# Kernel tuning notes

Hardware: AMD Instinct MI355X
Metric: run time of the kernel (lower is better)

## Reference

```python
import jax, jax.numpy as jnp
import numpy as np

NLAYERS, NHEADS, NFEAT, HDIM = 2, 8, 512, 64
ALPHA = 0.2
NEG = -9e15


def setup_inputs() -> dict:
    key = jax.random.key(0)
    ks = jax.random.split(key, 20)
    B, Ng, Nc, Nq = 4, 1024, 1024, 256
    s = 0.05
    inp = {
        "gloss": jax.random.normal(ks[0], (B, Ng, NFEAT), jnp.float32),
        "clip": jax.random.normal(ks[1], (B, Nc, NFEAT), jnp.float32),
        "question": jax.random.normal(ks[2], (B, Nq, NFEAT), jnp.float32),
        "gloss2clipadj": jax.random.randint(ks[3], (B, Ng, Nc), 0, 2, jnp.int32),
        "gloss2questionadj": jax.random.randint(ks[4], (B, Ng, Nq), 0, 2, jnp.int32),
    }
    # per-layer, per-head attention params: W [L,H,F,D], a split halves a1/a2 [L,H,D]
    for i, name in enumerate(["c2g", "g2q", "q2g"]):
        inp[name + "_W"] = jax.random.normal(ks[5 + i], (NLAYERS, NHEADS, NFEAT, HDIM), jnp.float32) * s
        inp[name + "_a1"] = jax.random.normal(ks[8 + i], (NLAYERS, NHEADS, HDIM), jnp.float32) * s
        inp[name + "_a2"] = jax.random.normal(ks[11 + i], (NLAYERS, NHEADS, HDIM), jnp.float32) * s
    # 4 FusionLayers per encoder layer (G2C, C2G, G2Q, Q2G), each with W,U,Wf,Uf [F,F]
    for i, name in enumerate(["fus_W", "fus_U", "fus_Wf", "fus_Uf"]):
        inp[name] = jax.random.normal(ks[14 + i], (NLAYERS, 4, NFEAT, NFEAT), jnp.float32) * s
    return inp


def _attn(q, kv, adj, W, a1, a2):
    # multi-head GAT-style additive cross attention; W [H,F,D], q [B,N,F], kv [B,M,F], adj [B,N,M]
    Wq = jnp.einsum('bnf,hfd->bhnd', q, W)
    Wk = jnp.einsum('bmf,hfd->bhmd', kv, W)
    e = jax.nn.leaky_relu(
        jnp.einsum('bhnd,hd->bhn', Wq, a1)[:, :, :, None]
        + jnp.einsum('bhmd,hd->bhm', Wk, a2)[:, :, None, :], ALPHA)
    e = jnp.where(adj[:, None, :, :] > 0, e, NEG)
    att = jax.nn.softmax(e, axis=2)  # torch F.softmax(dim=1) on [B,N,M]: query axis (faithful)
    h = jax.nn.elu(jnp.einsum('bhnm,bhmd->bhnd', att, Wk))
    B, H, N, D = h.shape
    return jnp.transpose(h, (0, 2, 1, 3)).reshape(B, N, H * D)  # concat heads


def _fusion(a, b, W, U, Wf, Uf):
    new_a = a @ W + b @ U
    f = jax.nn.sigmoid(a @ Wf + b @ Uf)
    return f * new_a + (1.0 - f) * a  # dropout is identity at inference


def reference(gloss, clip, question, gloss2clipadj, gloss2questionadj,
              c2g_W, c2g_a1, c2g_a2, g2q_W, g2q_a1, g2q_a2, q2g_W, q2g_a1, q2g_a2,
              fus_W, fus_U, fus_Wf, fus_Uf):
    g2c_f = gloss2clipadj.astype(gloss.dtype)
    g2q_T = jnp.transpose(gloss2questionadj, (0, 2, 1))
    for l in range(NLAYERS):
        gloss_same = jnp.einsum('bnm,bnf->bmf', g2c_f, gloss)  # adj^T @ gloss
        clip_1 = _fusion(clip, gloss_same, fus_W[l, 0], fus_U[l, 0], fus_Wf[l, 0], fus_Uf[l, 0])
        clip_agg = _attn(gloss, clip, gloss2clipadj, c2g_W[l], c2g_a1[l], c2g_a2[l])
        gloss_1 = _fusion(gloss, clip_agg, fus_W[l, 1], fus_U[l, 1], fus_Wf[l, 1], fus_Uf[l, 1])
        gloss_agg = _attn(question, gloss, g2q_T, g2q_W[l], g2q_a1[l], g2q_a2[l])
        question_1 = _fusion(question, gloss_agg, fus_W[l, 2], fus_U[l, 2], fus_Wf[l, 2], fus_Uf[l, 2])
        question_agg = _attn(gloss, question, gloss2questionadj, q2g_W[l], q2g_a1[l], q2g_a2[l])
        gloss_2 = _fusion(gloss_1, question_agg, fus_W[l, 3], fus_U[l, 3], fus_Wf[l, 3], fus_Uf[l, 3])
        gloss, clip, question = gloss_2, clip_1, question_1
    return gloss, clip, question
```

## Files before the change

kernel.cpp:

```cpp
#include <hip/hip_runtime.h>
#include <math.h>

#define NFEAT 512
#define NHEADS 8
#define HDIM 64
#define NB 4
#define NG 1024
#define NC 1024
#define NQ 256
#define NEGV -9e15f
#define CHUNKS 16
#define FF ((size_t)NFEAT*NFEAT)
#define LSTR 36
#define SEG 2304

typedef _Float16 v8h __attribute__((ext_vector_type(8)));
typedef float v4f __attribute__((ext_vector_type(4)));
#define MFMA16(a,b,c) __builtin_amdgcn_mfma_f32_16x16x32_f16((a),(b),(c),0,0,0)

#define GLDS(g, l) __builtin_amdgcn_global_load_lds( \
    (__attribute__((address_space(1))) void*)(g), \
    (__attribute__((address_space(3))) void*)(l), 16, 0, 0)

__device__ __forceinline__ int ldsw(int row, int quad){
// ... 119 lines not shown
    int b = blockIdx.z;
    int c0 = blockIdx.x*64, g0 = blockIdx.y*64;
    __shared__ int sI[64][65];
    int tid = threadIdx.x;
    #pragma unroll
    for (int it = 0; it < 4; ++it){
        int idx = it*256 + tid;
        int r = idx >> 4, c4 = idx & 15;
        int4 v = *(const int4*)(adj + ((size_t)b*NG + g0 + r)*NC + c0 + c4*4);
        sI[r][c4*4+0]=v.x; sI[r][c4*4+1]=v.y; sI[r][c4*4+2]=v.z; sI[r][c4*4+3]=v.w;
    }
    __syncthreads();
    int wv = tid >> 6, lane = tid & 63;
    #pragma unroll
    for (int it = 0; it < 2; ++it){
        int idx = it*256 + tid;
        int dd = idx >> 3, c8 = idx & 7;
        ushort4 p0, p1;
        #pragma unroll
        for (int j = 0; j < 4; ++j) (&p0.x)[j] = sI[c8*8+j][dd] > 0 ? (unsigned short)0x3C00 : (unsigned short)0;
        #pragma unroll
        for (int j = 0; j < 4; ++j) (&p1.x)[j] = sI[c8*8+4+j][dd] > 0 ? (unsigned short)0x3C00 : (unsigned short)0;
        unsigned short* o = dst + ((size_t)b*NC + c0 + dd)*NG + g0 + c8*8;
        *(ushort4*)o = p0; *(ushort4*)(o+4) = p1;
    }
    #pragma unroll
    for (int rr = wv; rr < 64; rr += 4){
        unsigned long long m = __ballot(sI[rr][lane] > 0);
        if (lane == 0) bm_gc[((size_t)b*NG + g0 + rr)*(NC/64) + (c0>>6)] = m;
    }
    #pragma unroll
    for (int cc = wv; cc < 64; cc += 4){
        unsigned long long m = __ballot(sI[lane][cc] > 0);
        if (lane == 0) bm_cg[((size_t)b*NC + c0 + cc)*(NG/64) + (g0>>6)] = m;
    }
}

__global__ __launch_bounds__(256) void adjT_int_k(const int* __restrict__ adj, int* __restrict__ dst,
    unsigned long long* __restrict__ bm_gq, unsigned long long* __restrict__ bm_qg){
    int b = blockIdx.z;
    int q0 = blockIdx.x*64, g0 = blockIdx.y*64;
    __shared__ int sI[64][65];
    int tid = threadIdx.x;
    #pragma unroll
    for (int it = 0; it < 4; ++it){
        int idx = it*256 + tid;
        int r = idx >> 4, c4 = idx & 15;
        int4 v = *(const int4*)(adj + ((size_t)b*NG + g0 + r)*NQ + q0 + c4*4);
        sI[r][c4*4+0]=v.x; sI[r][c4*4+1]=v.y; sI[r][c4*4+2]=v.z; sI[r][c4*4+3]=v.w;
    }
    __syncthreads();
    int wv = tid >> 6, lane = tid & 63;
    #pragma unroll
    for (int it = 0; it < 4; ++it){
        int idx = it*256 + tid;
        int dd = idx >> 4, c4 = idx & 15;
        int4 v{sI[c4*4+0][dd], sI[c4*4+1][dd], sI[c4*4+2][dd], sI[c4*4+3][dd]};
        *(int4*)(dst + ((size_t)b*NQ + q0 + dd)*NG + g0 + c4*4) = v;
    }
    #pragma unroll
    for (int rr = wv; rr < 64; rr += 4){
        unsigned long long m = __ballot(sI[rr][lane] > 0);
        if (lane == 0) bm_gq[((size_t)b*NG + g0 + rr)*(NQ/64) + (q0>>6)] = m;
    }
    #pragma unroll
    for (int cc = wv; cc < 64; cc += 4){
        unsigned long long m = __ballot(sI[lane][cc] > 0);
        if (lane == 0) bm_qg[((size_t)b*NQ + q0 + cc)*(NG/64) + (g0>>6)] = m;
    }
}

__global__ __launch_bounds__(256) void actT_hl_k(const float* __restrict__ src,
    unsigned short* __restrict__ dstHi, unsigned short* __restrict__ dstLo,
    unsigned short* __restrict__ rmHi, unsigned short* __restrict__ rmLo, int Nrows){
    int b = blockIdx.z;
    int f0 = blockIdx.x*64, g0 = blockIdx.y*64;
    __shared__ float sF[64][65];
    int tid = threadIdx.x;
    #pragma unroll
    for (int it = 0; it < 4; ++it){
        int idx = it*256 + tid;
        int r = idx >> 4, c4 = idx & 15;
        float4 v = *(const float4*)(src + ((size_t)b*Nrows + g0 + r)*512 + f0 + c4*4);
        sF[r][c4*4+0]=v.x; sF[r][c4*4+1]=v.y; sF[r][c4*4+2]=v.z; sF[r][c4*4+3]=v.w;
    }
    __syncthreads();
    #pragma unroll
    for (int it = 0; it < 2; ++it){
        int idx = it*256 + tid;
        int dd = idx >> 3, c8 = idx & 7;
        unsigned short hi[8], lo[8];
        #pragma unroll
        for (int j = 0; j < 8; ++j){
            float x = sF[c8*8+j][dd];
            hi[j] = f2h(x);
            lo[j] = f2h(x - h2f(hi[j]));
        }
        size_t oo = ((size_t)b*512 + f0 + dd)*Nrows + g0 + c8*8;
        *(ushort4*)(dstHi+oo)   = ushort4{hi[0],hi[1],hi[2],hi[3]};
        *(ushort4*)(dstHi+oo+4) = ushort4{hi[4],hi[5],hi[6],hi[7]};
        *(ushort4*)(dstLo+oo)   = ushort4{lo[0],lo[1],lo[2],lo[3]};
        *(ushort4*)(dstLo+oo+4) = ushort4{lo[4],lo[5],lo[6],lo[7]};
    }
    #pragma unroll
    for (int it = 0; it < 2; ++it){
        int idx = it*256 + tid;
        int r = idx >> 3, c8 = idx & 7;
        unsigned short hi[8], lo[8];
        #pragma unroll
        for (int j = 0; j < 8; ++j){
            float x = sF[r][c8*8+j];
            hi[j] = f2h(x);
            lo[j] = f2h(x - h2f(hi[j]));
        }
        size_t oo = ((size_t)b*Nrows + g0 + r)*512 + f0 + c8*8;
        *(ushort4*)(rmHi+oo)   = ushort4{hi[0],hi[1],hi[2],hi[3]};
        *(ushort4*)(rmHi+oo+4) = ushort4{hi[4],hi[5],hi[6],hi[7]};
        *(ushort4*)(rmLo+oo)   = ushort4{lo[0],lo[1],lo[2],lo[3]};
        *(ushort4*)(rmLo+oo+4) = ushort4{lo[4],lo[5],lo[6],lo[7]};
    }
}

__global__ __launch_bounds__(256) void scores3_k(
    const unsigned short* __restrict__ g, const unsigned short* __restrict__ c,
    const unsigned short* __restrict__ q,
    const float* __restrict__ wa13, const float* __restrict__ wa23,
    float* __restrict__ qs3, float* __restrict__ ks3){
    int lane = threadIdx.x & 63;
    int grow = blockIdx.x*4 + (threadIdx.x >> 6);
    int b = grow / 4608; int r = grow - b*4608;
    const unsigned short* X; const float* wa; float* out; int n, oOff, rowsX;
    if (r < SEG){
        out = qs3;
        if (r < 1024)      { X=g; wa=wa13;        n=r;        oOff=0;    rowsX=NG; }
        else if (r < 1280) { X=q; wa=wa13+4096;   n=r-1024;   oOff=1024; rowsX=NQ; }
        else               { X=g; wa=wa13+8192;   n=r-1280;   oOff=1280; rowsX=NG; }
    } else {
        out = ks3; r -= SEG;
        if (r < 1024)      { X=c; wa=wa23;        n=r;        oOff=0;    rowsX=NC; }
        else if (r < 2048) { X=g; wa=wa23+4096;   n=r-1024;   oOff=1024; rowsX=NG; }
        else               { X=q; wa=wa23+8192;   n=r-2048;   oOff=2048; rowsX=NQ; }
    }
    const unsigned short* Xr = X + ((size_t)b*rowsX + n)*NFEAT;
    float p[NHEADS];
    #pragma unroll
    for (int h = 0; h < NHEADS; ++h) p[h] = 0.f;
    #pragma unroll
    for (int cc = 0; cc < 8; ++cc){
        float x = h2f(Xr[(cc<<6) + lane]);
        #pragma unroll
        for (int h = 0; h < NHEADS; ++h) p[h] += x * wa[(h<<9) + (cc<<6) + lane];
    }
    #pragma unroll
    for (int h = 0; h < NHEADS; ++h){
        float v = p[h];
        #pragma unroll
        for (int off = 32; off > 0; off >>= 1) v += __shfl_xor(v, off);
        if (lane == 0) out[((size_t)b*SEG + oOff + n)*8 + h] = v;
    }
}

__global__ __launch_bounds__(256) void wkt3_mfma_k(
    const unsigned short* __restrict__ c, const unsigned short* __restrict__ g,
    const unsigned short* __restrict__ q, const unsigned short* __restrict__ WT3,
    unsigned short* __restrict__ WkT3){
    int b = blockIdx.z;
    int y = blockIdx.y;
    const unsigned short* kv; int rowsX, mOff, a;
    if (y < 16)      { a=0; kv=c; rowsX=NC; mOff=0; }
    else if (y < 32) { a=1; y-=16; kv=g; rowsX=NG; mOff=1024; }
    else             { a=2; y-=32; kv=q; rowsX=NQ; mOff=2048; }
    int r0 = y*64, c0 = blockIdx.x*64;
    int tid = threadIdx.x;
    __shared__ alignas(16) unsigned short aS[2][2048], bS[2][2048];
    const unsigned short* aG = kv + (size_t)b*rowsX*512;
    const unsigned short* bG = WT3 + (size_t)a*FF;
    int w = tid >> 6, lane = tid & 63;
    int lrow = lane & 15, quad = lane >> 4;
    int sr = tid >> 2;
    int sq = (tid & 3) ^ ((sr >> 1) & 3);
    size_t aRow = (size_t)(r0 + sr)*512 + sq*8;
    size_t bRow = (size_t)(c0 + sr)*512 + sq*8;
    v4f acc[4];
    #pragma unroll
    for (int cf = 0; cf < 4; ++cf) acc[cf] = (v4f)0.f;
    GLDS(aG + aRow, &aS[0][w << 9]);
    GLDS(bG + bRow, &bS[0][w << 9]);
    __syncthreads();
    int buf = 0;
    for (int s = 0; s < 16; ++s){
        if (s < 15){
            int ktn = (s + 1) << 5;
            GLDS(aG + aRow + ktn, &aS[buf^1][w << 9]);
            GLDS(bG + bRow + ktn, &bS[buf^1][w << 9]);
        }
        v8h af = *(const v8h*)&aS[buf][ldsw(w*16 + lrow, quad)];
        #pragma unroll
        for (int cf = 0; cf < 4; ++cf){
            v8h bf = *(const v8h*)&bS[buf][ldsw(cf*16 + lrow, quad)];
            acc[cf] = MFMA16(af, bf, acc[cf]);
        }
        __syncthreads();
        buf ^= 1;
    }
    #pragma unroll
    for (int cf = 0; cf < 4; ++cf){
        int colg = c0 + cf*16 + lrow;
        int rbase = r0 + w*16 + quad*4;
        ushort4 pk{f2h(acc[cf][0]), f2h(acc[cf][1]), f2h(acc[cf][2]), f2h(acc[cf][3])};
        *(ushort4*)&WkT3[((size_t)b*512 + colg)*SEG + mOff + rbase] = pk;
    }
}

__global__ __launch_bounds__(256) void colstat3_k(
    const unsigned* __restrict__ bm_cg, const unsigned* __restrict__ bm_gq,
    const unsigned* __restrict__ bm_qg,
    const float* __restrict__ qs3, const float* __restrict__ ks3,
    float* __restrict__ pcm, float* __restrict__ psum){
    int x = blockIdx.x, b = blockIdx.z;
    const unsigned* bm; int Mrows, N, N32, mOff, qOff;
    if (x < 256)      { bm=bm_cg; Mrows=NC; N=NG; N32=NG/32; mOff=0;    qOff=0; }
    else if (x < 512) { x-=256; bm=bm_gq; Mrows=NG; N=NQ; N32=NQ/32; mOff=1024; qOff=1024; }
    else              { x-=512; bm=bm_qg; Mrows=NQ; N=NG; N32=NG/32; mOff=2048; qOff=1280; }
    int mt = x >> 4, ch = x & 15;
    int chunk = N / CHUNKS, subl = chunk >> 2;
    int ml = threadIdx.x & 63; int m = mt*64 + ml;
    int g = threadIdx.x >> 6;
    int n0 = ch*chunk + g*subl;
    __shared__ float sQ[64][8];
    for (int t2 = threadIdx.x; t2 < chunk*8; t2 += 256)
        sQ[t2>>3][t2&7] = qs3[((size_t)b*SEG + qOff + ch*chunk)*8 + t2];
    float ksv[8];
    size_t mo = ((size_t)b*SEG + mOff + m)*8;
    #pragma unroll
    for (int h = 0; h < 8; ++h) ksv[h] = ks3[mo+h];
    unsigned word = bm[((size_t)b*Mrows + m)*N32 + (n0>>5)];
    unsigned bits = (word >> (n0 & 31)) & ((1u << subl) - 1u);
    __syncthreads();
    int nb = g*subl;
    float mx[8];
    #pragma unroll
    for (int h = 0; h < 8; ++h) mx[h] = -INFINITY;
    for (int i = 0; i < subl; ++i){
        if ((bits >> i) & 1){
            #pragma unroll
            for (int h = 0; h < 8; ++h) mx[h] = fmaxf(mx[h], sQ[nb+i][h]);
        }
    }
    float cm[8], s[8];
    #pragma unroll
    for (int h = 0; h < 8; ++h){
        cm[h] = bits ? lrelu(mx[h] + ksv[h]) : NEGV;
        s[h] = 0.f;
    }
    for (int i = 0; i < subl; ++i){
        bool on = (bits >> i) & 1;
        #pragma unroll
        for (int h = 0; h < 8; ++h){
            float e = on ? lrelu(sQ[nb+i][h] + ksv[h]) : NEGV;
            s[h] += __expf(e - cm[h]);
        }
    }
    __shared__ float scm[4][64][8], ssm[4][64][8];
    #pragma unroll
    for (int h = 0; h < 8; ++h){ scm[g][ml][h] = cm[h]; ssm[g][ml][h] = s[h]; }
    __syncthreads();
    if (g == 0){
        #pragma unroll
        for (int h = 0; h < 8; ++h){
            float c0 = scm[0][ml][h], c1 = scm[1][ml][h], c2 = scm[2][ml][h], c3 = scm[3][ml][h];
            float CM = fmaxf(fmaxf(c0, c1), fmaxf(c2, c3));
            float S = ssm[0][ml][h]*__expf(c0-CM) + ssm[1][ml][h]*__expf(c1-CM)
                    + ssm[2][ml][h]*__expf(c2-CM) + ssm[3][ml][h]*__expf(c3-CM);
            size_t o = (((size_t)b*CHUNKS + ch)*SEG + mOff + m)*8 + h;
            pcm[o] = CM; psum[o] = S;
        }
    }
}

__global__ __launch_bounds__(256) void colfin3_k(const float* __restrict__ pcm, const float* __restrict__ psum,
    const float* __restrict__ ks3, float* __restrict__ ksh, float* __restrict__ cmh,
    float* __restrict__ ish){
    int idx = blockIdx.x*256 + threadIdx.x;
    const int m8 = SEG*8;
    int b = idx / m8, rem = idx - b*m8;
    int m = rem >> 3, h = rem & 7;
    size_t base = (size_t)b*CHUNKS*m8 + rem;
    float c[CHUNKS], s[CHUNKS];
    #pragma unroll
    for (int ch = 0; ch < CHUNKS; ++ch){
        c[ch] = pcm[base + (size_t)ch*m8];
        s[ch] = psum[base + (size_t)ch*m8];
    }
    float CM = c[0];
    #pragma unroll
    for (int ch = 1; ch < CHUNKS; ++ch) CM = fmaxf(CM, c[ch]);
    float S = 0.f;
    #pragma unroll
    for (int ch = 0; ch < CHUNKS; ++ch) S += s[ch]*__expf(c[ch] - CM);
    size_t o = ((size_t)b*8 + h)*SEG + m;
    ksh[o] = ks3[idx]; cmh[o] = CM; ish[o] = 1.f/S;
}

__global__ __launch_bounds__(256) void fusion3_k(
    const unsigned short* __restrict__ aHi, const unsigned short* __restrict__ aLo,
    const unsigned short* __restrict__ bHi, const unsigned short* __restrict__ bLo,
    const unsigned short* __restrict__ Whi, const unsigned short* __restrict__ Wlo,
    unsigned short* __restrict__ dst, unsigned short* __restrict__ dstLo,
    unsigned short* __restrict__ dstT, unsigned short* __restrict__ dstTLo,
    float* __restrict__ dstF, int rows){
    int nY = rows >> 6;
    int ppg = (nY * NB) >> 3;
    int F = blockIdx.x;
    int xcd = F & 7, t = F >> 3;
    int c0i = t / ppg;
    int p = xcd + ((t - c0i*ppg) << 3);
    int r0 = (p % nY) << 6, c0 = c0i << 6;
    int b = p / nY;
    int tid = threadIdx.x;
    __shared__ alignas(16) unsigned short aHs[2048], bHs[2048], aLs[2048], bLs[2048];
    __shared__ alignas(16) unsigned short wHs[8192], wLs[8192];
    size_t actOff = (size_t)b*rows*512;
    const unsigned short* aHG = aHi + actOff;
    const unsigned short* bHG = bHi + actOff;
    const unsigned short* aLG = aLo ? aLo + actOff : nullptr;
    const unsigned short* bLG = bLo ? bLo + actOff : nullptr;
    bool hasALo = (aLG != nullptr);
    bool hasBLo = (bLG != nullptr);
    int w = tid >> 6, lane = tid & 63;
    int wr = w >> 1, wc = w & 1;
    int lrow = lane & 15, quad = lane >> 4;
    int sr = tid >> 2;
    int sq = (tid & 3) ^ ((sr >> 1) & 3);
    size_t aRow = (size_t)(r0 + sr)*512 + sq*8;
    size_t wPk = (size_t)c0i*16*8192 + (size_t)sr*32 + sq*8;
    unsigned short* ldsA  = &aHs[w << 9];
    unsigned short* ldsB  = &bHs[w << 9];
    unsigned short* ldsAL = &aLs[w << 9];
    unsigned short* ldsBL = &bLs[w << 9];
    v4f accN[2][2], accF[2][2];
    #pragma unroll
    for (int r = 0; r < 2; ++r)
        #pragma unroll
        for (int cf = 0; cf < 2; ++cf){ accN[r][cf] = (v4f)0.f; accF[r][cf] = (v4f)0.f; }
    for (int kt = 0; kt < 512; kt += 32){
        __syncthreads();
        GLDS(aHG + aRow + kt, ldsA);
        GLDS(bHG + aRow + kt, ldsB);
        if (hasALo) GLDS(aLG + aRow + kt, ldsAL);
        if (hasBLo) GLDS(bLG + aRow + kt, ldsBL);
        size_t wk = wPk + (size_t)(kt >> 5)*8192;
        #pragma unroll
        for (int m = 0; m < 4; ++m){
            GLDS(Whi + wk + (m<<11), &wHs[(m<<11) + (w<<9)]);
            GLDS(Wlo + wk + (m<<11), &wLs[(m<<11) + (w<<9)]);
        }
        __syncthreads();
        v8h ah[2], bh[2], al[2], bl[2];
        #pragma unroll
        for (int r = 0; r < 2; ++r){
            int ao = ldsw(wr*32 + r*16 + lrow, quad);
            ah[r] = *(const v8h*)&aHs[ao];
            bh[r] = *(const v8h*)&bHs[ao];
            if (hasALo) al[r] = *(const v8h*)&aLs[ao];
            if (hasBLo) bl[r] = *(const v8h*)&bLs[ao];
        }
        #pragma unroll
        for (int cf = 0; cf < 2; ++cf){
            int wo = ldsw(wc*32 + cf*16 + lrow, quad);
            v8h w0 = *(const v8h*)&wHs[wo];
            v8h w1 = *(const v8h*)&wHs[2048 + wo];
            v8h w2 = *(const v8h*)&wHs[4096 + wo];
            v8h w3 = *(const v8h*)&wHs[6144 + wo];
            v8h l0 = *(const v8h*)&wLs[wo];
            v8h l1 = *(const v8h*)&wLs[2048 + wo];
            v8h l2 = *(const v8h*)&wLs[4096 + wo];
            v8h l3 = *(const v8h*)&wLs[6144 + wo];
            #pragma unroll
            for (int r = 0; r < 2; ++r){
                accN[r][cf] = MFMA16(ah[r], w0, accN[r][cf]);
                accN[r][cf] = MFMA16(bh[r], w1, accN[r][cf]);
                accF[r][cf] = MFMA16(ah[r], w2, accF[r][cf]);
                accF[r][cf] = MFMA16(bh[r], w3, accF[r][cf]);
                if (hasALo){ accN[r][cf] = MFMA16(al[r], w0, accN[r][cf]); accF[r][cf] = MFMA16(al[r], w2, accF[r][cf]); }
                if (hasBLo){ accN[r][cf] = MFMA16(bl[r], w1, accN[r][cf]); accF[r][cf] = MFMA16(bl[r], w3, accF[r][cf]); }
                accN[r][cf] = MFMA16(ah[r], l0, accN[r][cf]);
                accN[r][cf] = MFMA16(bh[r], l1, accN[r][cf]);
                accF[r][cf] = MFMA16(ah[r], l2, accF[r][cf]);
                accF[r][cf] = MFMA16(bh[r], l3, accF[r][cf]);
            }
        }
    }
    #pragma unroll
    for (int r = 0; r < 2; ++r)
        #pragma unroll
        for (int cf = 0; cf < 2; ++cf){
            int colg = c0 + wc*32 + cf*16 + lrow;
            int rbase = r0 + wr*32 + r*16 + quad*4;
            float o4[4];
            #pragma unroll
            for (int reg = 0; reg < 4; ++reg){
                float f = 1.f/(1.f + __expf(-accF[r][cf][reg]));
                size_t ai = (size_t)(rbase+reg)*512 + colg;
                float ao = h2f(aHG[ai]);
                if (aLG) ao += h2f(aLG[ai]);
                o4[reg] = f*accN[r][cf][reg] + (1.f - f)*ao;
                size_t oo = ((size_t)b*rows + rbase + reg)*512 + colg;
                unsigned short hv = f2h(o4[reg]);
                dst[oo] = hv;
                if (dstLo) dstLo[oo] = f2h(o4[reg] - h2f(hv));
                if (dstF) dstF[oo] = o4[reg];
            }
            if (dstT){
                unsigned short h0 = f2h(o4[0]), h1 = f2h(o4[1]), h2 = f2h(o4[2]), h3 = f2h(o4[3]);
                size_t to = ((size_t)b*512 + colg)*rows + rbase;
                *(ushort4*)&dstT[to] = ushort4{h0,h1,h2,h3};
                if (dstTLo)
                    *(ushort4*)&dstTLo[to] = ushort4{f2h(o4[0]-h2f(h0)), f2h(o4[1]-h2f(h1)),
                                                     f2h(o4[2]-h2f(h2)), f2h(o4[3]-h2f(h3))};
            }
        }
}

__global__ __launch_bounds__(256) void fusion1_k(
    const unsigned short* __restrict__ aHi, const unsigned short* __restrict__ aLo,
    const unsigned short* __restrict__ bHi,
    const unsigned short* __restrict__ Whi,
    unsigned short* __restrict__ dst, unsigned short* __restrict__ dstLo,
    float* __restrict__ dstF, int rows){
    int nY = rows >> 6;
    int ppg = (nY * NB) >> 3;
    int F = blockIdx.x;
    int xcd = F & 7, t = F >> 3;
    int c0i = t / ppg;
    int p = xcd + ((t - c0i*ppg) << 3);
    int r0 = (p % nY) << 6, c0 = c0i << 6;
    int b = p / nY;
    int tid = threadIdx.x;
    __shared__ alignas(16) unsigned short aHs[2][2048], bHs[2][2048];
    __shared__ alignas(16) unsigned short wHs[2][8192];
    size_t actOff = (size_t)b*rows*512;
    const unsigned short* aHG = aHi + actOff;
    const unsigned short* bHG = bHi + actOff;
    const unsigned short* aLG = aLo ? aLo + actOff : nullptr;
    int w = tid >> 6, lane = tid & 63;
    int wr = w >> 1, wc = w & 1;
    int lrow = lane & 15, quad = lane >> 4;
    int sr = tid >> 2;
    int sq = (tid & 3) ^ ((sr >> 1) & 3);
    size_t aRow = (size_t)(r0 + sr)*512 + sq*8;
    size_t wPk = (size_t)c0i*16*8192 + (size_t)sr*32 + sq*8;
    v4f accN[2][2], accF[2][2];
    #pragma unroll
    for (int r = 0; r < 2; ++r)
        #pragma unroll
        for (int cf = 0; cf < 2; ++cf){ accN[r][cf] = (v4f)0.f; accF[r][cf] = (v4f)0.f; }

    #define F1STAGE(bb, kk) do{ \
        GLDS(aHG + aRow + (kk), &aHs[bb][w << 9]); \
        GLDS(bHG + aRow + (kk), &bHs[bb][w << 9]); \
        size_t wk_ = wPk + (size_t)((kk) >> 5)*8192; \
        GLDS(Whi + wk_,          &wHs[bb][(0<<11) + (w<<9)]); \
        GLDS(Whi + wk_ + (1<<11), &wHs[bb][(1<<11) + (w<<9)]); \
        GLDS(Whi + wk_ + (2<<11), &wHs[bb][(2<<11) + (w<<9)]); \
        GLDS(Whi + wk_ + (3<<11), &wHs[bb][(3<<11) + (w<<9)]); \
    } while(0)

    F1STAGE(0, 0);
    __syncthreads();
    int buf = 0;
    for (int kt = 0; kt < 512; kt += 32){
        if (kt + 32 < 512) F1STAGE(buf^1, kt + 32);
        v8h ah[2], bh[2];
        #pragma unroll
        for (int r = 0; r < 2; ++r){
            int ao = ldsw(wr*32 + r*16 + lrow, quad);
            ah[r] = *(const v8h*)&aHs[buf][ao];
            bh[r] = *(const v8h*)&bHs[buf][ao];
        }
        #pragma unroll
        for (int cf = 0; cf < 2; ++cf){
            int wo = ldsw(wc*32 + cf*16 + lrow, quad);
            v8h w0 = *(const v8h*)&wHs[buf][wo];
            v8h w1 = *(const v8h*)&wHs[buf][2048 + wo];
            v8h w2 = *(const v8h*)&wHs[buf][4096 + wo];
            v8h w3 = *(const v8h*)&wHs[buf][6144 + wo];
            #pragma unroll
            for (int r = 0; r < 2; ++r){
                accN[r][cf] = MFMA16(ah[r], w0, accN[r][cf]);
                accN[r][cf] = MFMA16(bh[r], w1, accN[r][cf]);
                accF[r][cf] = MFMA16(ah[r], w2, accF[r][cf]);
                accF[r][cf] = MFMA16(bh[r], w3, accF[r][cf]);
            }
        }
        __syncthreads();
        buf ^= 1;
    }
    #undef F1STAGE
    #pragma unroll
    for (int r = 0; r < 2; ++r)
        #pragma unroll
        for (int cf = 0; cf < 2; ++cf){
            int colg = c0 + wc*32 + cf*16 + lrow;
            int rbase = r0 + wr*32 + r*16 + quad*4;
            #pragma unroll
            for (int reg = 0; reg < 4; ++reg){
                float f = 1.f/(1.f + __expf(-accF[r][cf][reg]));
                size_t ai = (size_t)(rbase+reg)*512 + colg;
                float ao = h2f(aHG[ai]);
                if (aLG) ao += h2f(aLG[ai]);
                float o = f*accN[r][cf][reg] + (1.f - f)*ao;
                size_t oo = ((size_t)b*rows + rbase + reg)*512 + colg;
                unsigned short hv = f2h(o);
                dst[oo] = hv;
                if (dstLo) dstLo[oo] = f2h(o - h2f(hv));
                if (dstF) dstF[oo] = o;
            }
        }
}

__global__ __launch_bounds__(256) void gemmT_mfma_k(
    const unsigned short* __restrict__ A, size_t aStride,
    const unsigned short* __restrict__ BT, const unsigned short* __restrict__ BT2, size_t bStride,
    int K, int rowsPB,
    unsigned short* __restrict__ outRM, unsigned short* __restrict__ outLo,
    unsigned short* __restrict__ outT){
    int b = blockIdx.z;
    int r0 = blockIdx.y*64, c0 = blockIdx.x*64;
    int tid = threadIdx.x;
    __shared__ alignas(16) unsigned short aS[2][2048], bS[2][2048];
    const unsigned short* aG = A + (size_t)b*aStride;
    const unsigned short* bG0 = BT + (size_t)b*bStride;
    const unsigned short* bG1 = BT2 ? BT2 + (size_t)b*bStride : nullptr;
    int w = tid >> 6, lane = tid & 63;
    int lrow = lane & 15, quad = lane >> 4;
    int sr = tid >> 2;
    int sq = (tid & 3) ^ ((sr >> 1) & 3);
    size_t aRow = (size_t)(r0 + sr)*K + sq*8;
    size_t bRow = (size_t)(c0 + sr)*K + sq*8;
    int spp = K >> 5;
    int nsteps = (BT2 ? 2 : 1)*spp;
    v4f acc[4];
    #pragma unroll
    for (int cf = 0; cf < 4; ++cf) acc[cf] = (v4f)0.f;
    GLDS(aG + aRow, &aS[0][w << 9]);
    GLDS(bG0 + bRow, &bS[0][w << 9]);
    __syncthreads();
    int buf = 0;
    for (int s = 0; s < nsteps; ++s){
        int sn = s + 1;
        if (sn < nsteps){
            int ktn = ((sn >= spp) ? (sn - spp) : sn) << 5;
            const unsigned short* bgn = (sn >= spp) ? bG1 : bG0;
            GLDS(aG + aRow + ktn, &aS[buf^1][w << 9]);
            GLDS(bgn + bRow + ktn, &bS[buf^1][w << 9]);
        }
        v8h af = *(const v8h*)&aS[buf][ldsw(w*16 + lrow, quad)];
        #pragma unroll
        for (int cf = 0; cf < 4; ++cf){
            v8h bf = *(const v8h*)&bS[buf][ldsw(cf*16 + lrow, quad)];
            acc[cf] = MFMA16(af, bf, acc[cf]);
        }
        __syncthreads();
        buf ^= 1;
    }
    #pragma unroll
    for (int cf = 0; cf < 4; ++cf){
        int colg = c0 + cf*16 + lrow;
        int rbase = r0 + w*16 + quad*4;
        if (outRM){
            #pragma unroll
            for (int reg = 0; reg < 4; ++reg){
                float v = acc[cf][reg];
                unsigned short hv = f2h(v);
                size_t oo = ((size_t)b*rowsPB + rbase + reg)*512 + colg;
                outRM[oo] = hv;
                if (outLo) outLo[oo] = f2h(v - h2f(hv));
            }
        }
        if (outT){
            ushort4 pk{f2h(acc[cf][0]), f2h(acc[cf][1]), f2h(acc[cf][2]), f2h(acc[cf][3])};
            *(ushort4*)&outT[((size_t)b*512 + colg)*rowsPB + rbase] = pk;
        }
    }
}

__global__ __launch_bounds__(256) void attn_mfma_k(const unsigned* __restrict__ bmN, int M32,
    const float* __restrict__ qs3, int qOff,
    const float* __restrict__ ksh, const float* __restrict__ cmh, const float* __restrict__ ish,
    int mOff, const unsigned short* __restrict__ WkT3,
    unsigned short* __restrict__ outp, int N, int M){
    int nN0 = N >> 6;
    int F = blockIdx.x;
    int xcd = F & 7, t = F >> 3;
    int bh = xcd*4 + t/nN0;
    int n0 = (t % nN0) << 6;
    int b = bh >> 3, h = bh & 7;
    int tid = threadIdx.x;
    __shared__ unsigned short pS[2*64*LSTR];
    __shared__ alignas(16) unsigned short wS[2*2048];
    __shared__ float qsS[64];
    __shared__ alignas(16) float sKs[1024], sCm[1024], sIs[1024];
    const float* ksb = ksh + ((size_t)b*8 + h)*SEG + mOff;
    const float* cmb = cmh + ((size_t)b*8 + h)*SEG + mOff;
    const float* isb = ish + ((size_t)b*8 + h)*SEG + mOff;
    const unsigned short* wkb = WkT3 + ((size_t)b*512 + h*64)*SEG + mOff;
    int w = tid >> 6, lane = tid & 63;
    int lrow = lane & 15, quad = lane >> 4;
    int pn = tid >> 2, pm = (tid & 3)*8;
    int sr = tid >> 2;
    int sq = (tid & 3) ^ ((sr >> 1) & 3);
    for (int o = w*256; o < M; o += 1024){
        GLDS(ksb + o + lane*4, &sKs[o]);
        GLDS(cmb + o + lane*4, &sCm[o]);
        GLDS(isb + o + lane*4, &sIs[o]);
    }
    if (tid < 64) qsS[tid] = qs3[((size_t)b*SEG + qOff + n0 + tid)*8 + h];
    const unsigned* bmrow = bmN + ((size_t)b*N + n0 + pn)*M32;
    v4f acc[4];
    #pragma unroll
    for (int cf = 0; cf < 4; ++cf) acc[cf] = (v4f)0.f;
    uint2 CW = *(const uint2*)(bmrow);
    uint2 NW;
    __syncthreads();
    float qv = qsS[pn];
    for (int mt = 0; mt < M; mt += 64){
        int mtB = mt + 32;
        int mtN = (mt + 64 < M) ? (mt + 64) : 0;
        GLDS(wkb + (size_t)sr*SEG + mt + sq*8, &wS[w << 9]);
        {
            unsigned bb = (CW.x >> pm) & 0xffu;
            float4 k0 = *(const float4*)&sKs[mt+pm], k1 = *(const float4*)&sKs[mt+pm+4];
            float4 c0 = *(const float4*)&sCm[mt+pm], c1 = *(const float4*)&sCm[mt+pm+4];
            float4 i0 = *(const float4*)&sIs[mt+pm], i1 = *(const float4*)&sIs[mt+pm+4];
            float p[8];
            const float* kk0 = &k0.x; const float* kk1 = &k1.x;
            const float* cc0 = &c0.x; const float* cc1 = &c1.x;
            const float* ii0 = &i0.x; const float* ii1 = &i1.x;
            #pragma unroll
            for (int j = 0; j < 4; ++j){
                float e = ((bb >> j) & 1) ? lrelu(qv + kk0[j]) : NEGV;
                p[j] = __expf(e - cc0[j]) * ii0[j];
            }
            #pragma unroll
            for (int j = 0; j < 4; ++j){
                float e = ((bb >> (4+j)) & 1) ? lrelu(qv + kk1[j]) : NEGV;
                p[4+j] = __expf(e - cc1[j]) * ii1[j];
            }
            *(ushort4*)&pS[pn*LSTR + pm]     = ushort4{f2h(p[0]), f2h(p[1]), f2h(p[2]), f2h(p[3])};
            *(ushort4*)&pS[pn*LSTR + pm + 4] = ushort4{f2h(p[4]), f2h(p[5]), f2h(p[6]), f2h(p[7])};
        }
        __syncthreads();
        {
            v8h af = *(const v8h*)&pS[(w*16 + lrow)*LSTR + quad*8];
            #pragma unroll
            for (int cf = 0; cf < 4; ++cf){
                v8h bf = *(const v8h*)&wS[ldsw(cf*16 + lrow, quad)];
                acc[cf] = MFMA16(af, bf, acc[cf]);
            }
        }
        GLDS(wkb + (size_t)sr*SEG + mtB + sq*8, &wS[2048 + (w << 9)]);
        NW = *(const uint2*)(bmrow + (mtN >> 5));
        {
            unsigned bb = (CW.y >> pm) & 0xffu;
            float4 k0 = *(const float4*)&sKs[mtB+pm], k1 = *(const float4*)&sKs[mtB+pm+4];
            float4 c0 = *(const float4*)&sCm[mtB+pm], c1 = *(const float4*)&sCm[mtB+pm+4];
            float4 i0 = *(const float4*)&sIs[mtB+pm], i1 = *(const float4*)&sIs[mtB+pm+4];
            float p[8];
            const float* kk0 = &k0.x; const float* kk1 = &k1.x;
            const float* cc0 = &c0.x; const float* cc1 = &c1.x;
            const float* ii0 = &i0.x; const float* ii1 = &i1.x;
            #pragma unroll
            for (int j = 0; j < 4; ++j){
                float e = ((bb >> j) & 1) ? lrelu(qv + kk0[j]) : NEGV;
                p[j] = __expf(e - cc0[j]) * ii0[j];
            }
            #pragma unroll
            for (int j = 0; j < 4; ++j){
                float e = ((bb >> (4+j)) & 1) ? lrelu(qv + kk1[j]) : NEGV;
                p[4+j] = __expf(e - cc1[j]) * ii1[j];
            }
            *(ushort4*)&pS[2304 + pn*LSTR + pm]     = ushort4{f2h(p[0]), f2h(p[1]), f2h(p[2]), f2h(p[3])};
            *(ushort4*)&pS[2304 + pn*LSTR + pm + 4] = ushort4{f2h(p[4]), f2h(p[5]), f2h(p[6]), f2h(p[7])};
        }
        __syncthreads();
        {
            v8h af = *(const v8h*)&pS[2304 + (w*16 + lrow)*LSTR + quad*8];
            #pragma unroll
            for (int cf = 0; cf < 4; ++cf){
                v8h bf = *(const v8h*)&wS[2048 + ldsw(cf*16 + lrow, quad)];
                acc[cf] = MFMA16(af, bf, acc[cf]);
            }
        }
        CW = NW;
    }
    #pragma unroll
    for (int cf = 0; cf < 4; ++cf){
        int colg = h*64 + cf*16 + lrow;
        int rbase = n0 + w*16 + quad*4;
        #pragma unroll
        for (int reg = 0; reg < 4; ++reg){
            float v = acc[cf][reg];
            v = (v > 0.f) ? v : (__expf(v) - 1.f);
            outp[((size_t)b*N + rbase + reg)*512 + colg] = f2h(v);
        }
    }
}

extern "C" void kernel_launch(void* const* d_in, const int* in_sizes, int n_in,
                              void* d_out, int out_size, void* d_ws, size_t ws_size,
                              hipStream_t stream){
    const float* in_gloss = (const float*)d_in[0];
    const float* in_clip  = (const float*)d_in[1];
    const float* in_q     = (const float*)d_in[2];
    const int*   adj_gc   = (const int*)d_in[3];
    const int*   adj_gq   = (const int*)d_in[4];
    const float* c2gW  = (const float*)d_in[5];
    const float* c2ga1 = (const float*)d_in[6];
    const float* c2ga2 = (const float*)d_in[7];
    const float* g2qW  = (const float*)d_in[8];
    const float* g2qa1 = (const float*)d_in[9];
    const float* g2qa2 = (const float*)d_in[10];
    const float* q2gW  = (const float*)d_in[11];
    const float* q2ga1 = (const float*)d_in[12];
    const float* q2ga2 = (const float*)d_in[13];
    const float* fusW  = (const float*)d_in[14];
    const float* fusU  = (const float*)d_in[15];
    const float* fusWf = (const float*)d_in[16];
    const float* fusUf = (const float*)d_in[17];
    float* out = (float*)d_out;
    float* out_gloss = out;
    float* out_clip  = out + (size_t)NB*NG*NFEAT;
    float* out_q     = out + (size_t)NB*NG*NFEAT*2;

    char* wsB = (char*)d_ws;
    size_t off = 0;
    auto alloc = [&](size_t bytes){ void* p = wsB + off; off += (bytes + 255) & ~(size_t)255; return p; };
    float* wa13  = (float*)alloc(3*4096*4);
    float* wa23  = (float*)alloc(3*4096*4);
    float* qs3   = (float*)alloc((size_t)NB*SEG*8*4);
    float* ks3   = (float*)alloc((size_t)NB*SEG*8*4);
    float* ksh3  = (float*)alloc((size_t)NB*8*SEG*4);
    float* cmh3  = (float*)alloc((size_t)NB*8*SEG*4);
    float* ish3  = (float*)alloc((size_t)NB*8*SEG*4);
    float* pcm   = (float*)alloc((size_t)NB*CHUNKS*SEG*8*4);
    float* psum  = (float*)alloc((size_t)NB*CHUNKS*SEG*8*4);
    unsigned short* WflatT3 = (unsigned short*)alloc((size_t)3*FF*2);
    unsigned short* WkT3    = (unsigned short*)alloc((size_t)NB*512*SEG*2);
    unsigned short* wtAll   = (unsigned short*)alloc((size_t)32*FF*2);
    unsigned short* wtAllLo = (unsigned short*)alloc((size_t)32*FF*2);
    unsigned short* adjTgc  = (unsigned short*)alloc((size_t)NB*NC*NG*2);
    unsigned short* g_bf0   = (unsigned short*)alloc((size_t)NB*NG*NFEAT*2);
    unsigned short* gLo0    = (unsigned short*)alloc((size_t)NB*NG*NFEAT*2);
    unsigned short* g_bf1   = (unsigned short*)alloc((size_t)NB*NG*NFEAT*2);
    unsigned short* gLo1    = (unsigned short*)alloc((size_t)NB*NG*NFEAT*2);
    unsigned short* gT      = (unsigned short*)alloc((size_t)NB*NFEAT*NG*2);
    unsigned short* gTlo    = (unsigned short*)alloc((size_t)NB*NFEAT*NG*2);
    unsigned short* gA_bf   = (unsigned short*)alloc((size_t)NB*NG*NFEAT*2);
    unsigned short* gALo    = (unsigned short*)alloc((size_t)NB*NG*NFEAT*2);
    unsigned short* c_bf0   = (unsigned short*)alloc((size_t)NB*NC*NFEAT*2);
    unsigned short* cLo0    = (unsigned short*)alloc((size_t)NB*NC*NFEAT*2);
    unsigned short* c_bf1   = (unsigned short*)alloc((size_t)NB*NC*NFEAT*2);
    unsigned short* cLo1    = (unsigned short*)alloc((size_t)NB*NC*NFEAT*2);
    unsigned short* q_bf0   = (unsigned short*)alloc((size_t)NB*NQ*NFEAT*2);
    unsigned short* q_bf1   = (unsigned short*)alloc((size_t)NB*NQ*NFEAT*2);
    unsigned short* agg_bf  = (unsigned short*)alloc((size_t)NB*NG*NFEAT*2);
    unsigned short* aggLo   = (unsigned short*)alloc((size_t)NB*NG*NFEAT*2);
    int* adjTgq = (int*)alloc((size_t)NB*NQ*NG*4);
    unsigned* bm_gc = (unsigned*)alloc((size_t)NB*NG*(NC/32)*4);
    unsigned* bm_cg = (unsigned*)alloc((size_t)NB*NC*(NG/32)*4);
    unsigned* bm_gq = (unsigned*)alloc((size_t)NB*NG*(NQ/32)*4);
    unsigned* bm_qg = (unsigned*)alloc((size_t)NB*NQ*(NG/32)*4);
    (void)ws_size; (void)in_sizes; (void)n_in; (void)out_size;

    const size_t HFD = (size_t)NHEADS*NFEAT*HDIM;
    const size_t HD  = (size_t)NHEADS*HDIM;

    wtT_k<<<2048, 256, 0, stream>>>(fusW, fusU, fusWf, fusUf, wtAll, wtAllLo);
    adjT_h_k<<<dim3(NC/64, NG/64, NB), 256, 0, stream>>>(adj_gc, adjTgc,
        (unsigned long long*)bm_gc, (unsigned long long*)bm_cg);
    adjT_int_k<<<dim3(NQ/64, NG/64, NB), 256, 0, stream>>>(adj_gq, adjTgq,
        (unsigned long long*)bm_gq, (unsigned long long*)bm_qg);
    cvt_hl_k<<<(NB*NC*NFEAT)/2048, 256, 0, stream>>>(in_clip,  c_bf0, cLo0);
    cvt_h_k<<<(NB*NQ*NFEAT)/2048, 256, 0, stream>>>(in_q,     q_bf0);
    actT_hl_k<<<dim3(8, NG/64, NB), 256, 0, stream>>>(in_gloss, gT, gTlo, g_bf0, gLo0, NG);

    auto run_fusion = [&](const unsigned short* a, const unsigned short* aLo,
                          const unsigned short* bb, const unsigned short* bLo, int rows,
                          int l, int i, int npass,
                          unsigned short* dst, unsigned short* dstLo,
                          unsigned short* dstT, unsigned short* dstTLo, float* dstF){
        const unsigned short* Whi = wtAll   + (size_t)((l*4 + i)*4)*FF;
        const unsigned short* Wlo = wtAllLo + (size_t)((l*4 + i)*4)*FF;
        if (npass == 3)
            fusion3_k<<<dim3(8*(rows/64)*NB), 256, 0, stream>>>(
                a, aLo, bb, bLo, Whi, Wlo, dst, dstLo, dstT, dstTLo, dstF, rows);
        else
            fusion1_k<<<dim3(8*(rows/64)*NB), 256, 0, stream>>>(
                a, aLo, bb, Whi, dst, dstLo, dstF, rows);
    };

    for (int l = 0; l < 2; ++l){
        const unsigned short* g_cur = (l == 0) ? g_bf0 : g_bf1;
        const unsigned short* gLoC  = (l == 0) ? gLo0  : gLo1;
        const unsigned short* c_cur = (l == 0) ? c_bf0 : c_bf1;
        const unsigned short* cLoC  = (l == 0) ? cLo0  : cLo1;
        const unsigned short* q_cur = (l == 0) ? q_bf0 : q_bf1;
        unsigned short* g_nxt = (l == 0) ? g_bf1 : g_bf0;
        unsigned short* gLoN  = (l == 0) ? gLo1  : nullptr;
        unsigned short* c_nxt = (l == 0) ? c_bf1 : c_bf0;
        unsigned short* cLoN  = (l == 0) ? cLo1  : nullptr;
        unsigned short* q_nxt = (l == 0) ? q_bf1 : q_bf0;
        float* gF = (l == 1) ? out_gloss : nullptr;
        float* cF = (l == 1) ? out_clip  : nullptr;
        float* qF = (l == 1) ? out_q     : nullptr;

        prep_attnW3_k<<<240, 256, 0, stream>>>(
            c2gW + l*HFD, c2ga1 + l*HD, c2ga2 + l*HD,
            g2qW + l*HFD, g2qa1 + l*HD, g2qa2 + l*HD,
            q2gW + l*HFD, q2ga1 + l*HD, q2ga2 + l*HD,
            WflatT3, wa13, wa23);
        scores3_k<<<(NB*4608)/4, 256, 0, stream>>>(g_cur, c_cur, q_cur, wa13, wa23, qs3, ks3);
        wkt3_mfma_k<<<dim3(8, 36, NB), 256, 0, stream>>>(c_cur, g_cur, q_cur, WflatT3, WkT3);
        colstat3_k<<<dim3(576, 1, NB), 256, 0, stream>>>(bm_cg, bm_gq, bm_qg, qs3, ks3, pcm, psum);
        colfin3_k<<<(NB*SEG*8)/256, 256, 0, stream>>>(pcm, psum, ks3, ksh3, cmh3, ish3);

        gemmT_mfma_k<<<dim3(8, NC/64, NB), 256, 0, stream>>>(adjTgc, (size_t)NC*NG, gT, gTlo,
                                                             (size_t)512*NG, NG, NC,
                                                             agg_bf, aggLo, nullptr);
        run_fusion(c_cur, cLoC, agg_bf, aggLo, NC, l, 0, 3,
                   c_nxt, cLoN, nullptr, nullptr, cF);
        attn_mfma_k<<<(NG/64)*32, 256, 0, stream>>>(bm_gc, NC/32, qs3, 0, ksh3, cmh3, ish3, 0,
                                                    WkT3, agg_bf, NG, NC);
        run_fusion(g_cur, gLoC, agg_bf, nullptr, NG, l, 1, 1,
                   gA_bf, gALo, nullptr, nullptr, nullptr);
        attn_mfma_k<<<(NQ/64)*32, 256, 0, stream>>>(bm_qg, NG/32, qs3, 1024, ksh3, cmh3, ish3, 1024,
                                                    WkT3, agg_bf, NQ, NG);
        run_fusion(q_cur, nullptr, agg_bf, nullptr, NQ, l, 2, 1,
                   q_nxt, nullptr, nullptr, nullptr, qF);
        attn_mfma_k<<<(NG/64)*32, 256, 0, stream>>>(bm_gq, NQ/32, qs3, 1280, ksh3, cmh3, ish3, 2048,
                                                    WkT3, agg_bf, NG, NQ);
        run_fusion(gA_bf, gALo, agg_bf, nullptr, NG, l, 3, 3,
                   g_nxt, gLoN, (l == 0) ? gT : nullptr, (l == 0) ? gTlo : nullptr, gF);
    }
}
```

Measured before the change: 688.1 us.

## Batch independent attention and fusion launches into combined grid kernels

The three attention launches now run as one kernel that splits its grid by block index, with each attention writing to its own aggregate buffer. The four fusion launches are regrouped into two combined launches, one for the 1-pass fusions (gloss_1, question) and one for the 3-pass fusions (clip, gloss_2). The clip fusion moves after the attention so it can share a launch with the final gloss fusion. This removes launch gaps and tail underutilisation between small kernels, at the cost of extra aggregate buffers and a larger shared-memory footprint per combined kernel.

```diff
diff --git a/kernel.cpp b/kernel.cpp
--- a/kernel.cpp
+++ b/kernel.cpp
@@ -445,24 +445,23 @@
     ksh[o] = ks3[idx]; cmh[o] = CM; ish[o] = 1.f/S;
 }
 
-__global__ __launch_bounds__(256) void fusion3_k(
-    const unsigned short* __restrict__ aHi, const unsigned short* __restrict__ aLo,
-    const unsigned short* __restrict__ bHi, const unsigned short* __restrict__ bLo,
-    const unsigned short* __restrict__ Whi, const unsigned short* __restrict__ Wlo,
-    unsigned short* __restrict__ dst, unsigned short* __restrict__ dstLo,
-    unsigned short* __restrict__ dstT, unsigned short* __restrict__ dstTLo,
-    float* __restrict__ dstF, int rows){
+__device__ __forceinline__ void fusion3_body(int F,
+    unsigned short* aHs, unsigned short* bHs, unsigned short* aLs, unsigned short* bLs,
+    unsigned short* wHs, unsigned short* wLs,
+    const unsigned short* aHi, const unsigned short* aLo,
+    const unsigned short* bHi, const unsigned short* bLo,
+    const unsigned short* Whi, const unsigned short* Wlo,
+    unsigned short* dst, unsigned short* dstLo,
+    unsigned short* dstT, unsigned short* dstTLo,
+    float* dstF, int rows){
     int nY = rows >> 6;
     int ppg = (nY * NB) >> 3;
-    int F = blockIdx.x;
     int xcd = F & 7, t = F >> 3;
     int c0i = t / ppg;
     int p = xcd + ((t - c0i*ppg) << 3);
     int r0 = (p % nY) << 6, c0 = c0i << 6;
     int b = p / nY;
     int tid = threadIdx.x;
-    __shared__ alignas(16) unsigned short aHs[2048], bHs[2048], aLs[2048], bLs[2048];
-    __shared__ alignas(16) unsigned short wHs[8192], wLs[8192];
     size_t actOff = (size_t)b*rows*512;
     const unsigned short* aHG = aHi + actOff;
     const unsigned short* bHG = bHi + actOff;
@@ -565,23 +564,43 @@
         }
 }
 
-__global__ __launch_bounds__(256) void fusion1_k(
-    const unsigned short* __restrict__ aHi, const unsigned short* __restrict__ aLo,
-    const unsigned short* __restrict__ bHi,
-    const unsigned short* __restrict__ Whi,
-    unsigned short* __restrict__ dst, unsigned short* __restrict__ dstLo,
-    float* __restrict__ dstF, int rows){
+__global__ __launch_bounds__(256) void fusion3b_k(
+    const unsigned short* __restrict__ a0, const unsigned short* __restrict__ a0Lo,
+    const unsigned short* __restrict__ b0, const unsigned short* __restrict__ b0Lo,
+    const unsigned short* __restrict__ W0hi, const unsigned short* __restrict__ W0lo,
+    unsigned short* __restrict__ d0, unsigned short* __restrict__ d0Lo, float* __restrict__ d0F,
+    const unsigned short* __restrict__ a1, const unsigned short* __restrict__ a1Lo,
+    const unsigned short* __restrict__ b1,
+    const unsigned short* __restrict__ W1hi, const unsigned short* __restrict__ W1lo,
+    unsigned short* __restrict__ d1, unsigned short* __restrict__ d1Lo,
+    unsigned short* __restrict__ d1T, unsigned short* __restrict__ d1TLo, float* __restrict__ d1F){
+    __shared__ alignas(16) unsigned short aHs[2048], bHs[2048], aLs[2048], bLs[2048];
+    __shared__ alignas(16) unsigned short wHs[8192], wLs[8192];
+    int F = blockIdx.x;
+    const int S0 = 8*(NC/64)*NB;
+    if (F < S0)
+        fusion3_body(F, aHs, bHs, aLs, bLs, wHs, wLs,
+                     a0, a0Lo, b0, b0Lo, W0hi, W0lo,
+                     d0, d0Lo, nullptr, nullptr, d0F, NC);
+    else
+        fusion3_body(F - S0, aHs, bHs, aLs, bLs, wHs, wLs,
+                     a1, a1Lo, b1, nullptr, W1hi, W1lo,
+                     d1, d1Lo, d1T, d1TLo, d1F, NG);
+}
+
+__device__ __forceinline__ void fusion1_body(int F,
+    unsigned short (*aHs)[2048], unsigned short (*bHs)[2048], unsigned short (*wHs)[8192],
+    const unsigned short* aHi, const unsigned short* aLo,
+    const unsigned short* bHi, const unsigned short* Whi,
+    unsigned short* dst, unsigned short* dstLo, float* dstF, int rows){
     int nY = rows >> 6;
     int ppg = (nY * NB) >> 3;
-    int F = blockIdx.x;
     int xcd = F & 7, t = F >> 3;
     int c0i = t / ppg;
     int p = xcd + ((t - c0i*ppg) << 3);
     int r0 = (p % nY) << 6, c0 = c0i << 6;
     int b = p / nY;
     int tid = threadIdx.x;
-    __shared__ alignas(16) unsigned short aHs[2][2048], bHs[2][2048];
-    __shared__ alignas(16) unsigned short wHs[2][8192];
     size_t actOff = (size_t)b*rows*512;
     const unsigned short* aHG = aHi + actOff;
     const unsigned short* bHG = bHi + actOff;
@@ -660,6 +679,23 @@
                 if (dstF) dstF[oo] = o;
             }
         }
+}
+
+__global__ __launch_bounds__(256) void fusion1b_k(
+    const unsigned short* __restrict__ a0, const unsigned short* __restrict__ a0Lo,
+    const unsigned short* __restrict__ b0, const unsigned short* __restrict__ W0,
+    unsigned short* __restrict__ d0, unsigned short* __restrict__ d0Lo,
+    const unsigned short* __restrict__ a1, const unsigned short* __restrict__ b1,
+    const unsigned short* __restrict__ W1,
+    unsigned short* __restrict__ d1, float* __restrict__ d1F){
+    __shared__ alignas(16) unsigned short aHs[2][2048], bHs[2][2048];
+    __shared__ alignas(16) unsigned short wHs[2][8192];
+    int F = blockIdx.x;
+    const int S0 = 8*(NG/64)*NB;
+    if (F < S0)
+        fusion1_body(F, aHs, bHs, wHs, a0, a0Lo, b0, W0, d0, d0Lo, nullptr, NG);
+    else
+        fusion1_body(F - S0, aHs, bHs, wHs, a1, nullptr, b1, W1, d1, nullptr, d1F, NQ);
 }
 
 __global__ __launch_bounds__(256) void gemmT_mfma_k(
@@ -728,22 +764,19 @@
     }
 }
 
-__global__ __launch_bounds__(256) void attn_mfma_k(const unsigned* __restrict__ bmN, int M32,
-    const float* __restrict__ qs3, int qOff,
-    const float* __restrict__ ksh, const float* __restrict__ cmh, const float* __restrict__ ish,
-    int mOff, const unsigned short* __restrict__ WkT3,
-    unsigned short* __restrict__ outp, int N, int M){
+__device__ __forceinline__ void attn_body(int F,
+    unsigned short* pS, unsigned short* wS, float* qsS, float* sKs, float* sCm, float* sIs,
+    const unsigned* bmN, int M32,
+    const float* qs3, int qOff,
+    const float* ksh, const float* cmh, const float* ish,
+    int mOff, const unsigned short* WkT3,
+    unsigned short* outp, int N, int M){
     int nN0 = N >> 6;
-    int F = blockIdx.x;
     int xcd = F & 7, t = F >> 3;
     int bh = xcd*4 + t/nN0;
     int n0 = (t % nN0) << 6;
     int b = bh >> 3, h = bh & 7;
     int tid = threadIdx.x;
-    __shared__ unsigned short pS[2*64*LSTR];
-    __shared__ alignas(16) unsigned short wS[2*2048];
-    __shared__ float qsS[64];
-    __shared__ alignas(16) float sKs[1024], sCm[1024], sIs[1024];
     const float* ksb = ksh + ((size_t)b*8 + h)*SEG + mOff;
     const float* cmb = cmh + ((size_t)b*8 + h)*SEG + mOff;
     const float* isb = ish + ((size_t)b*8 + h)*SEG + mOff;
@@ -848,6 +881,32 @@
             outp[((size_t)b*N + rbase + reg)*512 + colg] = f2h(v);
         }
     }
+}
+
+__global__ __launch_bounds__(256) void attn_all_k(
+    const unsigned* __restrict__ bm_gc, const unsigned* __restrict__ bm_qg,
+    const unsigned* __restrict__ bm_gq,
+    const float* __restrict__ qs3,
+    const float* __restrict__ ksh, const float* __restrict__ cmh, const float* __restrict__ ish,
+    const unsigned short* __restrict__ WkT3,
+    unsigned short* __restrict__ agg0, unsigned short* __restrict__ agg1,
+    unsigned short* __restrict__ agg2){
+    __shared__ unsigned short pS[2*64*LSTR];
+    __shared__ alignas(16) unsigned short wS[2*2048];
+    __shared__ float qsS[64];
+    __shared__ alignas(16) float sKs[1024], sCm[1024], sIs[1024];
+    int F = blockIdx.x;
+    const int S0 = (NG/64)*32;
+    const int S1 = S0 + (NQ/64)*32;
+    if (F < S0)
+        attn_body(F, pS, wS, qsS, sKs, sCm, sIs, bm_gc, NC/32, qs3, 0,
+                  ksh, cmh, ish, 0, WkT3, agg0, NG, NC);
+    else if (F < S1)
+        attn_body(F - S0, pS, wS, qsS, sKs, sCm, sIs, bm_qg, NG/32, qs3, 1024,
+                  ksh, cmh, ish, 1024, WkT3, agg1, NQ, NG);
+    else
+        attn_body(F - S1, pS, wS, qsS, sKs, sCm, sIs, bm_gq, NQ/32, qs3, 1280,
+                  ksh, cmh, ish, 2048, WkT3, agg2, NG, NQ);
 }
 
 extern "C" void kernel_launch(void* const* d_in, const int* in_sizes, int n_in,
@@ -909,6 +968,9 @@
     unsigned short* q_bf1   = (unsigned short*)alloc((size_t)NB*NQ*NFEAT*2);
     unsigned short* agg_bf  = (unsigned short*)alloc((size_t)NB*NG*NFEAT*2);
     unsigned short* aggLo   = (unsigned short*)alloc((size_t)NB*NG*NFEAT*2);
+    unsigned short* agg0    = (unsigned short*)alloc((size_t)NB*NG*NFEAT*2);
+    unsigned short* agg1    = (unsigned short*)alloc((size_t)NB*NQ*NFEAT*2);
+    unsigned short* agg2    = (unsigned short*)alloc((size_t)NB*NG*NFEAT*2);
     int* adjTgq = (int*)alloc((size_t)NB*NQ*NG*4);
     unsigned* bm_gc = (unsigned*)alloc((size_t)NB*NG*(NC/32)*4);
     unsigned* bm_cg = (unsigned*)alloc((size_t)NB*NC*(NG/32)*4);
@@ -927,21 +989,6 @@
     cvt_hl_k<<<(NB*NC*NFEAT)/2048, 256, 0, stream>>>(in_clip,  c_bf0, cLo0);
     cvt_h_k<<<(NB*NQ*NFEAT)/2048, 256, 0, stream>>>(in_q,     q_bf0);
     actT_hl_k<<<dim3(8, NG/64, NB), 256, 0, stream>>>(in_gloss, gT, gTlo, g_bf0, gLo0, NG);
-
-    auto run_fusion = [&](const unsigned short* a, const unsigned short* aLo,
-                          const unsigned short* bb, const unsigned short* bLo, int rows,
-                          int l, int i, int npass,
-                          unsigned short* dst, unsigned short* dstLo,
-                          unsigned short* dstT, unsigned short* dstTLo, float* dstF){
-        const unsigned short* Whi = wtAll   + (size_t)((l*4 + i)*4)*FF;
-        const unsigned short* Wlo = wtAllLo + (size_t)((l*4 + i)*4)*FF;
-        if (npass == 3)
-            fusion3_k<<<dim3(8*(rows/64)*NB), 256, 0, stream>>>(
-                a, aLo, bb, bLo, Whi, Wlo, dst, dstLo, dstT, dstTLo, dstF, rows);
-        else
-            fusion1_k<<<dim3(8*(rows/64)*NB), 256, 0, stream>>>(
-                a, aLo, bb, Whi, dst, dstLo, dstF, rows);
-    };
 
     for (int l = 0; l < 2; ++l){
         const unsigned short* g_cur = (l == 0) ? g_bf0 : g_bf1;
@@ -971,19 +1018,17 @@
         gemmT_mfma_k<<<dim3(8, NC/64, NB), 256, 0, stream>>>(adjTgc, (size_t)NC*NG, gT, gTlo,
                                                              (size_t)512*NG, NG, NC,
                                                              agg_bf, aggLo, nullptr);
-        run_fusion(c_cur, cLoC, agg_bf, aggLo, NC, l, 0, 3,
-                   c_nxt, cLoN, nullptr, nullptr, cF);
-        attn_mfma_k<<<(NG/64)*32, 256, 0, stream>>>(bm_gc, NC/32, qs3, 0, ksh3, cmh3, ish3, 0,
-                                                    WkT3, agg_bf, NG, NC);
-        run_fusion(g_cur, gLoC, agg_bf, nullptr, NG, l, 1, 1,
-                   gA_bf, gALo, nullptr, nullptr, nullptr);
-        attn_mfma_k<<<(NQ/64)*32, 256, 0, stream>>>(bm_qg, NG/32, qs3, 1024, ksh3, cmh3, ish3, 1024,
-                                                    WkT3, agg_bf, NQ, NG);
-        run_fusion(q_cur, nullptr, agg_bf, nullptr, NQ, l, 2, 1,
-                   q_nxt, nullptr, nullptr, nullptr, qF);
-        attn_mfma_k<<<(NG/64)*32, 256, 0, stream>>>(bm_gq, NQ/32, qs3, 1280, ksh3, cmh3, ish3, 2048,
-                                                    WkT3, agg_bf, NG, NQ);
-        run_fusion(gA_bf, gALo, agg_bf, nullptr, NG, l, 3, 3,
-                   g_nxt, gLoN, (l == 0) ? gT : nullptr, (l == 0) ? gTlo : nullptr, gF);
-    }
-}
+        attn_all_k<<<(NG/64)*32 + (NQ/64)*32 + (NG/64)*32, 256, 0, stream>>>(
+            bm_gc, bm_qg, bm_gq, qs3, ksh3, cmh3, ish3, WkT3, agg0, agg1, agg2);
+        fusion1b_k<<<8*(NG/64)*NB + 8*(NQ/64)*NB, 256, 0, stream>>>(
+            g_cur, gLoC, agg0, wtAll + (size_t)((l*4 + 1)*4)*FF, gA_bf, gALo,
+            q_cur, agg1, wtAll + (size_t)((l*4 + 2)*4)*FF, q_nxt, qF);
+        fusion3b_k<<<8*(NC/64)*NB + 8*(NG/64)*NB, 256, 0, stream>>>(
+            c_cur, cLoC, agg_bf, aggLo,
+            wtAll + (size_t)((l*4 + 0)*4)*FF, wtAllLo + (size_t)((l*4 + 0)*4)*FF,
+            c_nxt, cLoN, cF,
+            gA_bf, gALo, agg2,
+            wtAll + (size_t)((l*4 + 3)*4)*FF, wtAllLo + (size_t)((l*4 + 3)*4)*FF,
+            g_nxt, gLoN, (l == 0) ? gT : nullptr, (l == 0) ? gTlo : nullptr, gF);
+    }
+}
```

After: 638.8 us. -7.2%, faster.
